# Kernel tuning notes

Hardware: AMD Instinct MI355X
Metric: run time of the kernel (lower is better)

Reference implementation:

```python
import jax, jax.numpy as jnp
import numpy as np

B, L, D = 4, 2048, 1024
N_HEADS = 16
D_KV = D // N_HEADS  # 64
TEMPERATURE = D_KV ** 0.5  # 8.0 (note: applied even though heads are never split)


def setup_inputs() -> dict:
    key = jax.random.key(0)
    ks = jax.random.split(key, 7)
    s = 1.0 / np.sqrt(D)
    return {
        "Q": jax.random.normal(ks[0], (B, L, D), jnp.float32),
        "K": jax.random.normal(ks[1], (B, L, D), jnp.float32),
        "V": jax.random.normal(ks[2], (B, L, D), jnp.float32),
        # nn.Linear weights, shape [out, in]; y = x @ W.T
        "W_Q": jax.random.normal(ks[3], (D, D), jnp.float32) * s,
        "W_K": jax.random.normal(ks[4], (D, D), jnp.float32) * s,
        "W_V": jax.random.normal(ks[5], (D, D), jnp.float32) * s,
        "W_O": jax.random.normal(ks[6], (D, D), jnp.float32) * s,
        "masked": 0,
    }


def reference(Q, K, V, W_Q, W_K, W_V, W_O, masked):
    # projections (no bias)
    q = jnp.einsum("bld,ed->ble", Q, W_Q)
    k = jnp.einsum("bld,ed->ble", K, W_K)
    v = jnp.einsum("bld,ed->ble", V, W_V)
    # NOTE: original module never splits heads; scores contract over full d_model
    scores = jnp.einsum("bqe,bke->bqk", q, k) / TEMPERATURE  # [B, L, L]
    if masked:
        # faithful (buggy) original: fill where tril is True
        tril = jnp.tril(jnp.ones((L, L), dtype=bool))
        scores = jnp.where(tril[None], -jnp.inf, scores)
    attn_weights = jax.nn.softmax(scores, axis=-1)
    # dropout(0.1) disabled (eval mode)
    x = jnp.einsum("bqk,bke->bqe", attn_weights, v)
    out = jnp.einsum("ble,de->bld", x, W_O)
    return (out, attn_weights)
```

## Files before the change

kernel.cpp:

```cpp
#include <hip/hip_runtime.h>
#include <math.h>


static constexpr int B_ = 4;
static constexpr int L_ = 2048;
static constexpr int D_ = 1024;

#define BM 128
#define BN 128
#define BKK 64

typedef _Float16 f16x8 __attribute__((ext_vector_type(8)));
typedef float    f32x4 __attribute__((ext_vector_type(4)));
typedef short    s16x8 __attribute__((ext_vector_type(8)));
typedef unsigned short u16x4 __attribute__((ext_vector_type(4)));

typedef __attribute__((address_space(1))) const unsigned int GU32;
typedef __attribute__((address_space(3))) unsigned int LU32;

__device__ __forceinline__ void gload_lds16(const void* g, void* l) {
    __builtin_amdgcn_global_load_lds((GU32*)g, (LU32*)l, 16, 0, 0);
}

__device__ __forceinline__ short f2h_bits(float x) {
    union { _Float16 h; short s; } u;
    u.h = (_Float16)x;
    return u.s;
}

__device__ __forceinline__ s16x8 cvt8h(float4 a, float4 b) {
    union { _Float16 h[8]; s16x8 s; } u;
    u.h[0] = (_Float16)a.x; u.h[1] = (_Float16)a.y;
    u.h[2] = (_Float16)a.z; u.h[3] = (_Float16)a.w;
    u.h[4] = (_Float16)b.x; u.h[5] = (_Float16)b.y;
    u.h[6] = (_Float16)b.z; u.h[7] = (_Float16)b.w;
    return u.s;
}

__device__ __forceinline__ void compute_step(
    const short* __restrict__ As, const short* __restrict__ Bs,
    int wr, int wc, int lr, int lk, f32x4 (&acc)[4][4])
{
#pragma unroll
    for (int kk = 0; kk < 2; ++kk) {
        const int slotk = kk * 4 + lk;
        f16x8 a[4], b[4];
#pragma unroll
        for (int m = 0; m < 4; ++m) {
            const int r = wr * 64 + m * 16 + lr;
            a[m] = *(const f16x8*)&As[r * 64 + ((slotk ^ (r & 7)) << 3)];
        }
#pragma unroll
        for (int n = 0; n < 4; ++n) {
            const int c = wc * 64 + n * 16 + lr;
            b[n] = *(const f16x8*)&Bs[c * 64 + ((slotk ^ (c & 7)) << 3)];
        }
#pragma unroll
        for (int m = 0; m < 4; ++m)
#pragma unroll
            for (int n = 0; n < 4; ++n)
                acc[m][n] = __builtin_amdgcn_mfma_f32_16x16x32_f16(a[m], b[n], acc[m][n], 0, 0, 0);
    }
}

template<int APPLY_SM>
__device__ __forceinline__ void epilogue_f16_bounce(
    short* __restrict__ lw, short* __restrict__ C, long N,
    int bm, int bn, int wr, int wc, int lr, int lk, int lane,
    const f32x4 (&acc)[4][4], float scale, bool msk)
{
#pragma unroll
    for (int m = 0; m < 4; ++m) {
        const int rl0 = m * 16 + lk * 4;
#pragma unroll
        for (int n = 0; n < 4; ++n) {
            const int cl = n * 16 + lr;
            const int slot = cl >> 3, cw = cl & 7;
#pragma unroll
            for (int g = 0; g < 4; ++g) {
                const int rl = rl0 + g;
                float v = acc[m][n][g];
                if constexpr (APPLY_SM) {
                    v *= scale;
                    if (msk && (bn + wc * 64 + cl) <= (bm + wr * 64 + rl)) v = -INFINITY;
                }
                lw[rl * 64 + ((slot ^ (rl & 7)) << 3) + cw] = f2h_bits(v);
            }
        }
    }
    const int l8 = lane & 7, lr8 = lane >> 3;
#pragma unroll
    for (int it = 0; it < 8; ++it) {
        const int rl = it * 8 + lr8;
        const int cl = (l8 ^ (rl & 7)) << 3;
        s16x8 d = *(const s16x8*)&lw[rl * 64 + (l8 << 3)];
        *(s16x8*)&C[(long)(bm + wr * 64 + rl) * N + bn + wc * 64 + cl] = d;
    }
}

__global__ __launch_bounds__(256) void proj_qkv(
    const short* __restrict__ qf, const short* __restrict__ kf, const short* __restrict__ vf,
    const short* __restrict__ wq, const short* __restrict__ wk, const short* __restrict__ wv,
    short* __restrict__ qh, short* __restrict__ kh, short* __restrict__ vT)
{
    __shared__ short smem[2 * BM * BKK];
    short* As = smem;
    short* Bs = smem + BM * BKK;

    const int t    = threadIdx.x;
    const int wid  = t >> 6;
    const int lane = t & 63;
    const int bz   = blockIdx.z;

    const short* A16 = (bz == 0) ? qf : (bz == 1) ? kf : vf;
    const short* Bt  = (bz == 0) ? wq : (bz == 1) ? wk : wv;

    const int gx = gridDim.x, gy = gridDim.y;
    const int wg = blockIdx.y * gx + blockIdx.x;
    const int bm = (wg % gy) * BM;
    const int bn = (wg / gy) * BN;

    const int wr = wid >> 1, wc = wid & 1;
    const int lr = lane & 15, lk = lane >> 4;
    const int srow = t >> 3, sslot = t & 7;
    const int K = D_;

    f32x4 acc[4][4];
#pragma unroll
    for (int m = 0; m < 4; ++m)
#pragma unroll
        for (int n = 0; n < 4; ++n) acc[m][n] = (f32x4)0.f;

    for (int k0 = 0; k0 < K; k0 += BKK) {
        __syncthreads();
#pragma unroll
        for (int i = 0; i < 4; ++i) {
            const int rb = i * 32 + srow;
            const short* g = Bt + (long)(bn + rb) * K + k0 + ((sslot ^ (rb & 7)) << 3);
            gload_lds16(g, &Bs[i * 2048 + wid * 512]);
        }
#pragma unroll
        for (int i = 0; i < 4; ++i) {
            const int ra = i * 32 + srow;
            const short* g = A16 + (long)(bm + ra) * K + k0 + ((sslot ^ (ra & 7)) << 3);
            gload_lds16(g, &As[i * 2048 + wid * 512]);
        }
        __syncthreads();
        compute_step(As, Bs, wr, wc, lr, lk, acc);
    }

    const int N = D_;
    if (bz < 2) {
        __syncthreads();
        short* C = (bz == 0) ? qh : kh;
        epilogue_f16_bounce<0>(smem + wid * 4096, C, N, bm, bn, wr, wc, lr, lk, lane,
                               acc, 1.f, false);
    } else {
#pragma unroll
        for (int m = 0; m < 4; ++m) {
            const int rg = bm + wr * 64 + m * 16 + lk * 4;
            const long rb = (long)(rg >> 11) * ((long)N * L_) + (rg & (L_ - 1));
#pragma unroll
            for (int n = 0; n < 4; ++n) {
                const int c = bn + wc * 64 + n * 16 + lr;
                u16x4 v;
#pragma unroll
                for (int g = 0; g < 4; ++g) v[g] = (unsigned short)f2h_bits(acc[m][n][g]);
                *(u16x4*)&vT[rb + (long)c * L_] = v;
            }
        }
    }
}

template<int OMODE>
__global__ __launch_bounds__(256) void hgemm(
    const short* __restrict__ A16p, const short* __restrict__ Btp, void* __restrict__ Cp_,
    int M, int N, int K, long sA, long sB, long sC,
    float scale, int useMask, const int* __restrict__ mflag)
{
    __shared__ short smem[2 * BM * BKK];
    short* As = smem;
    short* Bs = smem + BM * BKK;

    const int t    = threadIdx.x;
    const int wid  = t >> 6;
    const int lane = t & 63;
    const int bz   = blockIdx.z;

    const int gx = gridDim.x, gy = gridDim.y;
    const int wg = blockIdx.y * gx + blockIdx.x;
    const int bm = (wg % gy) * BM;
    const int bn = (wg / gy) * BN;

    const short* Bt  = Btp + (long)bz * sB;
    const short* A16 = A16p + (long)bz * sA;

    const int wr = wid >> 1, wc = wid & 1;
    const int lr = lane & 15, lk = lane >> 4;
    const int srow = t >> 3, sslot = t & 7;

    f32x4 acc[4][4];
#pragma unroll
    for (int m = 0; m < 4; ++m)
#pragma unroll
        for (int n = 0; n < 4; ++n) acc[m][n] = (f32x4)0.f;

    for (int k0 = 0; k0 < K; k0 += BKK) {
        __syncthreads();
#pragma unroll
        for (int i = 0; i < 4; ++i) {
            const int rb = i * 32 + srow;
            const short* g = Bt + (long)(bn + rb) * K + k0 + ((sslot ^ (rb & 7)) << 3);
            gload_lds16(g, &Bs[i * 2048 + wid * 512]);
        }
#pragma unroll
        for (int i = 0; i < 4; ++i) {
            const int ra = i * 32 + srow;
            const short* g = A16 + (long)(bm + ra) * K + k0 + ((sslot ^ (ra & 7)) << 3);
            gload_lds16(g, &As[i * 2048 + wid * 512]);
        }
        __syncthreads();
        compute_step(As, Bs, wr, wc, lr, lk, acc);
    }

    if constexpr (OMODE == 2) {
        float* C = (float*)Cp_ + (long)bz * sC;
#pragma unroll
        for (int m = 0; m < 4; ++m) {
            const int r0 = bm + wr * 64 + m * 16 + lk * 4;
#pragma unroll
            for (int n = 0; n < 4; ++n) {
                const int c = bn + wc * 64 + n * 16 + lr;
#pragma unroll
                for (int g = 0; g < 4; ++g)
                    C[(long)(r0 + g) * N + c] = acc[m][n][g] * scale;
            }
        }
    } else {
        __syncthreads();
        short* C = (short*)Cp_ + (long)bz * sC;
        const bool msk = (OMODE == 3) && useMask && (mflag[0] != 0);
        epilogue_f16_bounce<(OMODE == 3) ? 1 : 0>(
            smem + wid * 4096, C, N, bm, bn, wr, wc, lr, lk, lane, acc, scale, msk);
    }
}

__global__ __launch_bounds__(256) void cvt_w4_k(
    const float* __restrict__ W_Q, const float* __restrict__ W_K,
    const float* __restrict__ W_V, const float* __restrict__ W_O,
    short* __restrict__ dst)
{
    const int w = blockIdx.y;
    const float* src = (w == 0) ? W_Q : (w == 1) ? W_K : (w == 2) ? W_V : W_O;
    short* out = dst + (size_t)w * D_ * D_;
    const int i = blockIdx.x * 256 + threadIdx.x;
    float4 a = ((const float4*)src)[2 * i];
    float4 b = ((const float4*)src)[2 * i + 1];
    *(s16x8*)&out[i * 8] = cvt8h(a, b);
}

__global__ __launch_bounds__(256) void cvt_qkv_k(
    const float* __restrict__ Q, const float* __restrict__ K,
    const float* __restrict__ V, short* __restrict__ dst)
{
    const int w = blockIdx.y;
    const float* src = (w == 0) ? Q : (w == 1) ? K : V;
    short* out = dst + (size_t)w * B_ * L_ * D_;
    const int i = blockIdx.x * 256 + threadIdx.x;
    float4 a = ((const float4*)src)[2 * i];
    float4 b = ((const float4*)src)[2 * i + 1];
    *(s16x8*)&out[i * 8] = cvt8h(a, b);
}

__global__ __launch_bounds__(256) void softmax_rows_k(
    short* __restrict__ S16, float* __restrict__ Sout)
{
    const long row = blockIdx.x;
    short* p16 = S16 + row * (long)L_;
    float* pf  = Sout + row * (long)L_;
    const int tid = threadIdx.x;

    union { s16x8 v; _Float16 h[8]; } u;
    u.v = ((const s16x8*)p16)[tid];
    float f[8];
#pragma unroll
    for (int j = 0; j < 8; ++j) f[j] = (float)u.h[j];

    float m = f[0];
#pragma unroll
    for (int j = 1; j < 8; ++j) m = fmaxf(m, f[j]);
#pragma unroll
    for (int o = 32; o > 0; o >>= 1) m = fmaxf(m, __shfl_xor(m, o, 64));

    __shared__ float wmax[4], wsum[4];
    if ((tid & 63) == 0) wmax[tid >> 6] = m;
    __syncthreads();
    m = fmaxf(fmaxf(wmax[0], wmax[1]), fmaxf(wmax[2], wmax[3]));

    float s = 0.f;
#pragma unroll
    for (int j = 0; j < 8; ++j) { f[j] = expf(f[j] - m); s += f[j]; }
#pragma unroll
    for (int o = 32; o > 0; o >>= 1) s += __shfl_xor(s, o, 64);
    if ((tid & 63) == 0) wsum[tid >> 6] = s;
    __syncthreads();
    s = wsum[0] + wsum[1] + wsum[2] + wsum[3];

    const float inv = 1.f / s;
#pragma unroll
    for (int j = 0; j < 8; ++j) f[j] = f[j] * inv;

    float4 a, b;
    a.x = f[0]; a.y = f[1]; a.z = f[2]; a.w = f[3];
    b.x = f[4]; b.y = f[5]; b.z = f[6]; b.w = f[7];
    ((float4*)pf)[2 * tid]     = a;
    ((float4*)pf)[2 * tid + 1] = b;
    ((s16x8*)p16)[tid] = cvt8h(a, b);
}

extern "C" void kernel_launch(void* const* d_in, const int* in_sizes, int n_in,
                              void* d_out, int out_size, void* d_ws, size_t ws_size,
                              hipStream_t stream) {
    const float* Q   = (const float*)d_in[0];
    const float* K   = (const float*)d_in[1];
    const float* V   = (const float*)d_in[2];
    const float* W_Q = (const float*)d_in[3];
    const float* W_K = (const float*)d_in[4];
    const float* W_V = (const float*)d_in[5];
    const float* W_O = (const float*)d_in[6];
    const int* masked = (const int*)d_in[7];

    float* out  = (float*)d_out;
    float* attn = out + (size_t)B_ * L_ * D_;

    short* wq = (short*)d_ws;
    short* wk = wq + (size_t)D_ * D_;
    short* wv = wk + (size_t)D_ * D_;
    short* wo = wv + (size_t)D_ * D_;
    short* qh = wo + (size_t)D_ * D_;
    short* kh = qh + (size_t)B_ * L_ * D_;
    short* vT = kh + (size_t)B_ * L_ * D_;
    short* attn16 = vT + (size_t)B_ * L_ * D_;
    short* xh = qh;

    short* qf = (short*)attn;
    short* kf = qf + (size_t)B_ * L_ * D_;
    short* vf = kf + (size_t)B_ * L_ * D_;

    const long SLD = (long)L_ * D_;
    const long SLL = (long)L_ * L_;

    cvt_w4_k<<<dim3(D_ * D_ / 8 / 256, 4), 256, 0, stream>>>(W_Q, W_K, W_V, W_O, wq);
    cvt_qkv_k<<<dim3(B_ * L_ * D_ / 8 / 256, 3), 256, 0, stream>>>(Q, K, V, qf);

    proj_qkv<<<dim3(D_ / BN, (B_ * L_) / BM, 3), 256, 0, stream>>>(
        qf, kf, vf, wq, wk, wv, qh, kh, vT);

    dim3 gsc(L_ / BN, L_ / BM, B_);
    hgemm<3><<<gsc, 256, 0, stream>>>(qh, kh, attn16, L_, L_, D_, SLD, SLD, SLL,
                                      0.125f, 1, masked);

    softmax_rows_k<<<dim3(B_ * L_), 256, 0, stream>>>(attn16, attn);

    dim3 gav(D_ / BN, L_ / BM, B_);
    hgemm<0><<<gav, 256, 0, stream>>>(attn16, vT, xh, L_, D_, L_, SLL, SLD, SLD,
                                      1.f, 0, masked);

    dim3 gproj(D_ / BN, (B_ * L_) / BM, 1);
    hgemm<2><<<gproj, 256, 0, stream>>>(xh, wo, out, B_ * L_, D_, D_, 0, 0, 0,
                                        1.f, 0, masked);
}
```

Baseline: 254.6 us.

## Add 256x256-tile, 512-thread scores GEMM with 4-stage async LDS pipeline

Replaces the generic 128x128 hgemm for the QK^T scores with a dedicated kernel. It uses 256x256 output tiles, 8 waves each holding an 8x4 MFMA accumulator block, and a 4-buffer global_load_lds pipeline over K-steps of 32 with explicit vmcnt waits and s_setprio around the MFMA burst. The aim is more data reuse per tile and better overlap of loads with MFMA. In exchange, register pressure rises and the grid shrinks to 256 blocks, which may underfill the GPU's CUs. Scale and mask are applied in a new two-pass bounce epilogue.

```diff
diff --git a/kernel.cpp b/kernel.cpp
--- a/kernel.cpp
+++ b/kernel.cpp
@@ -36,6 +36,7 @@
     u.h[6] = (_Float16)b.z; u.h[7] = (_Float16)b.w;
     return u.s;
 }
+
 
 __device__ __forceinline__ void compute_step(
     const short* __restrict__ As, const short* __restrict__ Bs,
@@ -239,11 +240,157 @@
     } else {
         __syncthreads();
         short* C = (short*)Cp_ + (long)bz * sC;
-        const bool msk = (OMODE == 3) && useMask && (mflag[0] != 0);
-        epilogue_f16_bounce<(OMODE == 3) ? 1 : 0>(
-            smem + wid * 4096, C, N, bm, bn, wr, wc, lr, lk, lane, acc, scale, msk);
-    }
-}
+        epilogue_f16_bounce<0>(smem + wid * 4096, C, N, bm, bn, wr, wc, lr, lk, lane,
+                               acc, scale, false);
+    }
+}
+
+
+__device__ __forceinline__ void stage8(
+    const short* __restrict__ A16, const short* __restrict__ Bt,
+    short* __restrict__ As, short* __restrict__ Bs,
+    int bm, int bn, int k0, int K, int t, int wid)
+{
+    const int r0 = t >> 2;
+    const int sl = t & 3;
+#pragma unroll
+    for (int i = 0; i < 2; ++i) {
+        const int r = i * 128 + r0;
+        const short* g = A16 + (long)(bm + r) * K + k0 + ((sl ^ ((r >> 1) & 3)) << 3);
+        gload_lds16(g, As + i * 4096 + wid * 512);
+    }
+#pragma unroll
+    for (int i = 0; i < 2; ++i) {
+        const int r = i * 128 + r0;
+        const short* g = Bt + (long)(bn + r) * K + k0 + ((sl ^ ((r >> 1) & 3)) << 3);
+        gload_lds16(g, Bs + i * 4096 + wid * 512);
+    }
+}
+
+__device__ __forceinline__ void compute32(
+    const short* __restrict__ As, const short* __restrict__ Bs,
+    int wr, int wc, int lr, int lk, f32x4 (&acc)[8][4])
+{
+    f16x8 a[8], b[4];
+#pragma unroll
+    for (int m = 0; m < 8; ++m) {
+        const int r = wr * 128 + m * 16 + lr;
+        a[m] = *(const f16x8*)&As[r * 32 + ((lk ^ ((r >> 1) & 3)) << 3)];
+    }
+#pragma unroll
+    for (int n = 0; n < 4; ++n) {
+        const int c = wc * 64 + n * 16 + lr;
+        b[n] = *(const f16x8*)&Bs[c * 32 + ((lk ^ ((c >> 1) & 3)) << 3)];
+    }
+    __builtin_amdgcn_s_setprio(1);
+#pragma unroll
+    for (int m = 0; m < 8; ++m)
+#pragma unroll
+        for (int n = 0; n < 4; ++n)
+            acc[m][n] = __builtin_amdgcn_mfma_f32_16x16x32_f16(a[m], b[n], acc[m][n], 0, 0, 0);
+    __builtin_amdgcn_s_setprio(0);
+}
+
+template<int APPLY_SM>
+__device__ __forceinline__ void epilogue_f16_bounce8(
+    short* __restrict__ lw, short* __restrict__ C, long N,
+    int rowBase, int colBase, int lr, int lk, int lane,
+    const f32x4 (&acc)[8][4], float scale, bool msk)
+{
+#pragma unroll
+    for (int h = 0; h < 2; ++h) {
+#pragma unroll
+        for (int mm = 0; mm < 4; ++mm) {
+            const int m = h * 4 + mm;
+            const int rl0 = mm * 16 + lk * 4;
+#pragma unroll
+            for (int n = 0; n < 4; ++n) {
+                const int cl = n * 16 + lr;
+                const int slot = cl >> 3, cw = cl & 7;
+#pragma unroll
+                for (int g = 0; g < 4; ++g) {
+                    const int rl = rl0 + g;
+                    float v = acc[m][n][g];
+                    if constexpr (APPLY_SM) {
+                        v *= scale;
+                        if (msk && (colBase + cl) <= (rowBase + h * 64 + rl)) v = -INFINITY;
+                    }
+                    lw[rl * 64 + ((slot ^ (rl & 7)) << 3) + cw] = f2h_bits(v);
+                }
+            }
+        }
+        const int l8 = lane & 7, lr8 = lane >> 3;
+#pragma unroll
+        for (int it = 0; it < 8; ++it) {
+            const int rl = it * 8 + lr8;
+            const int cl = (l8 ^ (rl & 7)) << 3;
+            s16x8 d = *(const s16x8*)&lw[rl * 64 + (l8 << 3)];
+            *(s16x8*)&C[(long)(rowBase + h * 64 + rl) * N + colBase + cl] = d;
+        }
+    }
+}
+
+__global__ __launch_bounds__(512) void hgemm8_scores(
+    const short* __restrict__ qhp, const short* __restrict__ khp,
+    short* __restrict__ Cp, const int* __restrict__ mflag)
+{
+    __shared__ short smem[65536];
+
+    const int t    = threadIdx.x;
+    const int wid  = t >> 6;
+    const int lane = t & 63;
+    const int bz   = blockIdx.z;
+    const int K    = D_;
+
+    const int wg = blockIdx.y * 8 + blockIdx.x;
+    const int bm = (wg % 8) * 256;
+    const int bn = (wg / 8) * 256;
+
+    const short* A16 = qhp + (long)bz * L_ * D_;
+    const short* Bt  = khp + (long)bz * L_ * D_;
+    short* C = Cp + (long)bz * ((long)L_ * L_);
+
+    const int wr = wid >> 2, wc = wid & 3;
+    const int lr = lane & 15, lk = lane >> 4;
+
+    f32x4 acc[8][4];
+#pragma unroll
+    for (int m = 0; m < 8; ++m)
+#pragma unroll
+        for (int n = 0; n < 4; ++n) acc[m][n] = (f32x4)0.f;
+
+    short* Abuf = smem;
+    short* Bbuf = smem + 32768;
+
+    stage8(A16, Bt, Abuf + 0 * 8192, Bbuf + 0 * 8192, bm, bn, 0,  K, t, wid);
+    stage8(A16, Bt, Abuf + 1 * 8192, Bbuf + 1 * 8192, bm, bn, 32, K, t, wid);
+    stage8(A16, Bt, Abuf + 2 * 8192, Bbuf + 2 * 8192, bm, bn, 64, K, t, wid);
+
+    const int nt = K / 32;
+    for (int ti = 0; ti < nt; ++ti) {
+        if (ti + 2 < nt)      asm volatile("s_waitcnt vmcnt(8)" ::: "memory");
+        else if (ti + 1 < nt) asm volatile("s_waitcnt vmcnt(4)" ::: "memory");
+        else                  asm volatile("s_waitcnt vmcnt(0)" ::: "memory");
+        __builtin_amdgcn_sched_barrier(0);
+        __builtin_amdgcn_s_barrier();
+        __builtin_amdgcn_sched_barrier(0);
+        asm volatile("" ::: "memory");
+        if (ti + 3 < nt) {
+            const int nb = (ti + 3) & 3;
+            stage8(A16, Bt, Abuf + nb * 8192, Bbuf + nb * 8192, bm, bn,
+                   (ti + 3) * 32, K, t, wid);
+        }
+        const int cb = ti & 3;
+        compute32(Abuf + cb * 8192, Bbuf + cb * 8192, wr, wc, lr, lk, acc);
+    }
+    __syncthreads();
+
+    const bool msk = (mflag[0] != 0);
+    epilogue_f16_bounce8<1>(smem + wid * 4096, C, L_,
+                            bm + wr * 128, bn + wc * 64, lr, lk, lane,
+                            acc, 0.125f, msk);
+}
+
 
 __global__ __launch_bounds__(256) void cvt_w4_k(
     const float* __restrict__ W_Q, const float* __restrict__ W_K,
@@ -356,9 +503,7 @@
     proj_qkv<<<dim3(D_ / BN, (B_ * L_) / BM, 3), 256, 0, stream>>>(
         qf, kf, vf, wq, wk, wv, qh, kh, vT);
 
-    dim3 gsc(L_ / BN, L_ / BM, B_);
-    hgemm<3><<<gsc, 256, 0, stream>>>(qh, kh, attn16, L_, L_, D_, SLD, SLD, SLL,
-                                      0.125f, 1, masked);
+    hgemm8_scores<<<dim3(8, 8, B_), 512, 0, stream>>>(qh, kh, attn16, masked);
 
     softmax_rows_k<<<dim3(B_ * L_), 256, 0, stream>>>(attn16, attn);
 
```

Result: faster. 239.3 us (-6.0%).
